# Optimization experiments

Measured on AMD Instinct MI355X. Metric: run time of the kernel, lower is better.

## Reference

```python
import jax, jax.numpy as jnp
import numpy as np
from jax.scipy.special import gammaln, digamma, logsumexp

# Gauss-Legendre quadrature on [0, 0.5] for the regularized incomplete beta
# I_{0.5}(a, b) = (1/B(a,b)) * int_0^{0.5} t^{a-1} (1-t)^{b-1} dt
_Q = 256
_gx, _gw = np.polynomial.legendre.leggauss(_Q)
_T_NP = 0.25 * (_gx + 1.0)          # nodes mapped to (0, 0.5)
_LOGW_NP = np.log(0.25 * _gw)       # log of scaled weights (half-length 0.25)


def betainc_half(a, b):
    """Regularized incomplete beta I_{0.5}(a, b), vectorized over leading dims.
    Evaluated in log-space via fixed Gauss-Legendre quadrature so it is smooth
    and differentiable in (a, b) (mirrors the custom BetaInc.apply autograd op).
    a, b: [...] positive floats. Returns [...].
    """
    t = jnp.asarray(_T_NP, dtype=a.dtype)        # [Q]
    logw = jnp.asarray(_LOGW_NP, dtype=a.dtype)  # [Q]
    # [..., Q] log integrand
    log_int = logw + (a[..., None] - 1.0) * jnp.log(t) \
                   + (b[..., None] - 1.0) * jnp.log1p(-t)
    log_B = gammaln(a) + gammaln(b) - gammaln(a + b)
    return jnp.exp(logsumexp(log_int, axis=-1) - log_B)


def setup_inputs() -> dict:
    key = jax.random.key(0)
    k1, k2, k3 = jax.random.split(key, 3)
    B, V = 65536, 512
    post_log = 0.1 * jax.random.normal(k1, (V,), dtype=jnp.float32)  # post_ param
    prior = jnp.ones((V,), dtype=jnp.float32)                        # prior = 1.0
    out = (2 * jax.random.randint(k2, (B, V), 0, 2) - 1).astype(jnp.int32)  # voter preds in {-1,+1}
    y = (2 * jax.random.randint(k3, (B, 1), 0, 2) - 1).astype(jnp.int32)    # labels in {-1,+1}
    return {"post_log": post_log, "prior": prior, "out": out, "y": y}


def reference(post_log, prior, out, y):
    B = out.shape[0]
    post = jnp.exp(post_log)                      # [V]
    eq = (y == out).astype(post.dtype)            # [B, V]
    correct = eq @ post                           # sum of post where y == out
    wrong = (1.0 - eq) @ post                     # sum of post where y != out
    # exact margin: m = 1 - 2 * I_{0.5}(correct, wrong)
    margin = 1.0 - 2.0 * betainc_half(correct, wrong)[:, None]   # [B, 1]
    # KL(Dir(post) || Dir(prior))
    kl = gammaln(post.sum()) - gammaln(post).sum()
    kl = kl - (gammaln(prior.sum()) - gammaln(prior).sum())
    kl = kl + jnp.sum((post - prior) * (digamma(post) - digamma(post.sum())))
    # predict: one Dirichlet draw of voter weights, score per label in {-1, +1}
    mv_post = jax.random.dirichlet(jax.random.key(1), post).astype(post.dtype)  # [V]
    score_neg = ((out == -1).astype(post.dtype) @ mv_post)[:, None]  # [B, 1]
    score_pos = ((out == 1).astype(post.dtype) @ mv_post)[:, None]   # [B, 1]
    kl_col = kl * jnp.ones((B, 1), dtype=post.dtype)
    # columns: [margin, score(label=-1), score(label=+1), kl]
    return jnp.concatenate([margin, score_neg, score_pos, kl_col], axis=1)
```

## Files before the change

### kernel.cpp

```cpp
#include <hip/hip_runtime.h>
#include <math.h>


struct K2 { unsigned a, b; };

__device__ __forceinline__ unsigned rotl32(unsigned v, int r) {
  return (v << r) | (v >> (32 - r));
}

__device__ __forceinline__ K2 tf2x32(K2 k, unsigned x0, unsigned x1) {
  unsigned ks0 = k.a, ks1 = k.b, ks2 = k.a ^ k.b ^ 0x1BD11BDAu;
  x0 += ks0; x1 += ks1;
#define TF_ROUND(r) { x0 += x1; x1 = rotl32(x1, (r)); x1 ^= x0; }
  TF_ROUND(13) TF_ROUND(15) TF_ROUND(26) TF_ROUND(6)
  x0 += ks1; x1 += ks2 + 1u;
  TF_ROUND(17) TF_ROUND(29) TF_ROUND(16) TF_ROUND(24)
  x0 += ks2; x1 += ks0 + 2u;
  TF_ROUND(13) TF_ROUND(15) TF_ROUND(26) TF_ROUND(6)
  x0 += ks0; x1 += ks1 + 3u;
  TF_ROUND(17) TF_ROUND(29) TF_ROUND(16) TF_ROUND(24)
  x0 += ks1; x1 += ks2 + 4u;
  TF_ROUND(13) TF_ROUND(15) TF_ROUND(26) TF_ROUND(6)
  x0 += ks2; x1 += ks0 + 5u;
#undef TF_ROUND
  return {x0, x1};
}

__device__ __forceinline__ void split2f(K2& key, K2& sub) {
  K2 c = tf2x32(key, 0u, 0u);
  sub = tf2x32(key, 0u, 1u);
  key = c;
}

__device__ __forceinline__ void split3f(K2& key, K2& xk, K2& Uk) {
  K2 c = tf2x32(key, 0u, 0u);
  xk = tf2x32(key, 0u, 1u);
  Uk = tf2x32(key, 0u, 2u);
  key = c;
}

__device__ __forceinline__ K2 split512_at(K2 k, int i) {
  return tf2x32(k, 0u, (unsigned)i);
}

__device__ __forceinline__ unsigned rbits32(K2 k) {
  K2 r = tf2x32(k, 0u, 0u);
  return r.a ^ r.b;
}

__device__ __forceinline__ float bits_to_u01(unsigned bits) {
  unsigned fb = (bits >> 9) | 0x3F800000u;
  return __uint_as_float(fb) - 1.0f;
}

__device__ __forceinline__ float erfinv_xla(float x) {
#pragma clang fp contract(off)
  float w = -log1pf(-(x * x));
  float p;
  if (w < 5.0f) {
    w = w - 2.5f;
    p = 2.81022636e-08f;
    p = 3.43273939e-07f + p * w;
    p = -3.5233877e-06f + p * w;
    p = -4.39150654e-06f + p * w;
    p = 0.00021858087f + p * w;
    p = -0.00125372503f + p * w;
    p = -0.00417768164f + p * w;
    p = 0.246640727f + p * w;
    p = 1.50140941f + p * w;
  } else {
    w = sqrtf(w) - 3.0f;
    p = -0.000200214257f;
    p = 0.000100950558f + p * w;
    p = 0.00134934322f + p * w;
    p = -0.00367342844f + p * w;
    p = 0.00573950773f + p * w;
    p = -0.0076224613f + p * w;
    p = 0.00943887047f + p * w;
    p = 1.00167406f + p * w;
    p = 2.83297682f + p * w;
  }
  return p * x;
}

__device__ __forceinline__ float normal_from_key(K2 k) {
#pragma clang fp contract(off)
  const float lo = -0.99999994f;
  float f = bits_to_u01(rbits32(k));
  float u = f * 2.0f + lo;
  u = fmaxf(lo, u);
  return 1.41421356f * erfinv_xla(u);
}

__device__ float gamma_one_log(K2 key, float alpha) {
#pragma clang fp contract(off)
  float alpha_orig = alpha;
  bool boost = (alpha >= 1.0f);
  float al = boost ? alpha : (alpha + 1.0f);
  float d = al - 0.33333334f;
  float c = 0.33333334f / sqrtf(9.0f * d);
  K2 sub;
  split2f(key, sub);
  float u_boost = bits_to_u01(rbits32(sub));
  float X = 0.0f, V = 1.0f, U = 2.0f;
  while ((U >= 1.0f - 0.0331f * (X * X)) &&
         (logf(U) >= 0.5f * X + d * ((1.0f - V) + logf(V)))) {
    K2 xk, Uk;
    split3f(key, xk, Uk);
    float x = 0.0f, v = -1.0f;
    while (v <= 0.0f) {
      K2 s2;
      split2f(xk, s2);
      x = normal_from_key(s2);
      v = 1.0f + x * c;
    }
    X = x * x;
    V = (v * v) * v;
    U = bits_to_u01(rbits32(Uk));
  }
  float log_sample = logf(d) + logf(V);
  if (boost) return log_sample;
  return log_sample + log1pf(-u_boost) / alpha_orig;
}

__device__ __forceinline__ double digamma_d(double x) {
  double r = 0.0;
  while (x < 6.0) { r -= 1.0 / x; x += 1.0; }
  double f = 1.0 / (x * x);
  double ser = f * (1.0 / 12.0 -
               f * (1.0 / 120.0 -
               f * (1.0 / 252.0 -
               f * (1.0 / 240.0 -
               f * (1.0 / 132.0)))));
  return r + log(x) - 0.5 / x - ser;
}

__device__ __forceinline__ double lgamma_stir(double x) {
  double shift = 0.0;
  while (x < 8.0) { shift -= log(x); x += 1.0; }
  double f = 1.0 / (x * x);
  double ser = (1.0 / 12.0 -
               f * (1.0 / 360.0 -
               f * (1.0 / 1260.0 -
               f * (1.0 / 1680.0)))) / x;
  return shift + 0.918938533204672741780329736406 + (x - 0.5) * log(x) - x + ser;
}

__device__ double breduce_sum(double* sd, double v) {
  int t = threadIdx.x;
  sd[t] = v; __syncthreads();
  for (int s = 256; s > 0; s >>= 1) {
    if (t < s) sd[t] += sd[t + s];
    __syncthreads();
  }
  double r = sd[0]; __syncthreads();
  return r;
}

__device__ float breduce_maxf(float* sf, float v) {
  int t = threadIdx.x;
  sf[t] = v; __syncthreads();
  for (int s = 256; s > 0; s >>= 1) {
    if (t < s) sf[t] = fmaxf(sf[t], sf[t + s]);
    __syncthreads();
  }
  float r = sf[0]; __syncthreads();
  return r;
}

__device__ float breduce_sumf(float* sf, float v) {
  int t = threadIdx.x;
  sf[t] = v; __syncthreads();
  for (int s = 256; s > 0; s >>= 1) {
    if (t < s) sf[t] += sf[t + s];
    __syncthreads();
  }
  float r = sf[0]; __syncthreads();
  return r;
}

#define MTAB_N 16384

__global__ void __launch_bounds__(512) smv_setup_kernel(
    const float* __restrict__ post_log, const float* __restrict__ prior,
    unsigned char* __restrict__ ws) {
  double* wsd = (double*)ws;
  float* fbase = (float*)(ws + 64);
  float* postf = fbase;
  float* mvf = fbase + 512;
  float* mtab = fbase + 1792;
  int tid = threadIdx.x;
  __shared__ double sd[512];

  if (blockIdx.x == 0) {
    __shared__ float sf[512];
    float alpha = expf(post_log[tid]);
    postf[tid] = alpha;
    double p = (double)alpha;
    double S = breduce_sum(sd, p);

    K2 root = {0u, 1u};
    K2 kv = split512_at(root, tid);
    float lg = gamma_one_log(kv, alpha);
    float mx = breduce_maxf(sf, lg);
    float un = expf(lg - mx);
    float se = breduce_sumf(sf, un);
    float mvv = un / se;
    mvf[tid] = mvv;
    float mtot = breduce_sumf(sf, mvv);

    double pr = (double)prior[tid];
    double dgS = digamma_d(S);
    double t3 = (p - pr) * (digamma_d(p) - dgS);
    double sum_lgp = breduce_sum(sd, lgamma(p));
    double Spr = breduce_sum(sd, pr);
    double sum_lgpr = breduce_sum(sd, lgamma(pr));
    double sum_t3 = breduce_sum(sd, t3);
    if (tid == 0) {
      double kl = lgamma(S) - sum_lgp - (lgamma(Spr) - sum_lgpr) + sum_t3;
      wsd[0] = S;
      wsd[1] = lgamma(S);
      wsd[2] = kl;
      wsd[3] = (double)mtot;
    }
    return;
  }

  double S = breduce_sum(sd, (double)expf(post_log[tid]));
  double lgS = lgamma(S);

  __shared__ float slt[256], sl1t[256], slw[256];
  if (tid < 256) {
    const int n = 256;
    const double nn = (double)n;
    double th = M_PI * (tid + 0.75) / (nn + 0.5);
    double corr = 1.0 - 1.0 / (8.0 * nn * nn) + 1.0 / (8.0 * nn * nn * nn);
    double x = corr * cos(th);
    double p0 = 1.0, p1 = x;
    for (int k = 2; k <= n; ++k) {
      double pk = ((2.0 * k - 1.0) * x * p1 - (k - 1.0) * p0) / (double)k;
      p0 = p1; p1 = pk;
    }
    double dp = nn * (x * p1 - p0) / (x * x - 1.0);
    double dx = -p1 / dp;
    double d2p = (2.0 * x * dp - nn * (nn + 1.0) * p1) / (1.0 - x * x);
    double xn = x + dx;
    double dpn = dp + d2p * dx;
    double w = 2.0 / ((1.0 - xn * xn) * dpn * dpn);
    double t = 0.25 * (xn + 1.0);
    slt[tid] = (float)log(t);
    sl1t[tid] = (float)log1p(-t);
    slw[tid] = (float)log(0.25 * w);
  }
  __syncthreads();

  int idx = (blockIdx.x - 1) * 512 + tid;
  double ad = S * (double)idx / (double)(MTAB_N - 1);
  ad = fmin(fmax(ad, 0.05), S - 0.05);
  float a = (float)ad;
  float b = (float)(S - ad);
  float am1 = a - 1.0f, bm1 = b - 1.0f;

  float m = -1e30f, s = 0.0f;
  for (int q = 0; q < 256; ++q) {
    float le = slw[q] + am1 * slt[q] + bm1 * sl1t[q];
    if (le > m) {
      s = s * expf(m - le) + 1.0f;
      m = le;
    } else {
      s += expf(le - m);
    }
  }
  float lse = m + logf(s);
  double logB = lgamma_stir(ad) + lgamma_stir((double)(S - ad)) - lgS;
  double I = exp((double)lse - logB);
  mtab[idx] = (float)(1.0 - 2.0 * I);
}

__global__ void __launch_bounds__(512) smv_main_kernel(
    const int* __restrict__ vout, const int* __restrict__ y,
    const unsigned char* __restrict__ ws, float* __restrict__ dout, int B) {
  __shared__ float s_post[512], s_mv[512];
  const double* wsd = (const double*)ws;
  const float* fbase = (const float*)(ws + 64);
  const float* mtab = fbase + 1792;
  int tid = threadIdx.x;
  s_post[tid] = fbase[tid];
  s_mv[tid] = fbase[512 + tid];
  float Sf = (float)wsd[0];
  float Mtot = (float)wsd[3];
  float klf = (float)wsd[2];
  float scale = (float)(MTAB_N - 1) / Sf;
  __syncthreads();

  int wave = tid >> 6, lane = tid & 63;
  int r0 = (blockIdx.x * 8 + wave) * 4;
  if (r0 >= B) return;

  const int4* rp0 = (const int4*)(vout + (size_t)r0 * 512);
  const int4* rp1 = (const int4*)(vout + (size_t)min(r0 + 1, B - 1) * 512);
  const int4* rp2 = (const int4*)(vout + (size_t)min(r0 + 2, B - 1) * 512);
  const int4* rp3 = (const int4*)(vout + (size_t)min(r0 + 3, B - 1) * 512);

  int4 v00 = rp0[lane], v01 = rp0[64 + lane];
  int4 v10 = rp1[lane], v11 = rp1[64 + lane];
  int4 v20 = rp2[lane], v21 = rp2[64 + lane];
  int4 v30 = rp3[lane], v31 = rp3[64 + lane];

  float4 p0 = *(const float4*)&s_post[lane * 4];
  float4 m0 = *(const float4*)&s_mv[lane * 4];
  float4 p1 = *(const float4*)&s_post[256 + lane * 4];
  float4 m1 = *(const float4*)&s_mv[256 + lane * 4];

  float dP0 = 0.f, dM0 = 0.f, dP1 = 0.f, dM1 = 0.f;
  float dP2 = 0.f, dM2 = 0.f, dP3 = 0.f, dM3 = 0.f;

#define ACC(dP, dM, c, pp, mm)                        \
  {                                                   \
    float ox = (float)(c).x, oy = (float)(c).y,       \
          oz = (float)(c).z, ow = (float)(c).w;       \
    dP = fmaf(ox, (pp).x, dP); dM = fmaf(ox, (mm).x, dM); \
    dP = fmaf(oy, (pp).y, dP); dM = fmaf(oy, (mm).y, dM); \
    dP = fmaf(oz, (pp).z, dP); dM = fmaf(oz, (mm).z, dM); \
    dP = fmaf(ow, (pp).w, dP); dM = fmaf(ow, (mm).w, dM); \
  }
  ACC(dP0, dM0, v00, p0, m0) ACC(dP0, dM0, v01, p1, m1)
  ACC(dP1, dM1, v10, p0, m0) ACC(dP1, dM1, v11, p1, m1)
  ACC(dP2, dM2, v20, p0, m0) ACC(dP2, dM2, v21, p1, m1)
  ACC(dP3, dM3, v30, p0, m0) ACC(dP3, dM3, v31, p1, m1)
#undef ACC

#pragma unroll
  for (int m = 1; m < 64; m <<= 1) {
    dP0 += __shfl_xor(dP0, m); dM0 += __shfl_xor(dM0, m);
    dP1 += __shfl_xor(dP1, m); dM1 += __shfl_xor(dM1, m);
    dP2 += __shfl_xor(dP2, m); dM2 += __shfl_xor(dM2, m);
    dP3 += __shfl_xor(dP3, m); dM3 += __shfl_xor(dM3, m);
  }

  if (lane < 4) {
    int r = r0 + lane;
    if (r < B) {
      float dP = (lane == 0) ? dP0 : (lane == 1) ? dP1 : (lane == 2) ? dP2 : dP3;
      float dM = (lane == 0) ? dM0 : (lane == 1) ? dM1 : (lane == 2) ? dM2 : dM3;
      float cneg = (Sf - dP) * 0.5f;
      float mneg = (Mtot - dM) * 0.5f;
      int yr = y[r];
      float a = (yr == -1) ? cneg : (Sf - cneg);
      float x = a * scale;
      x = fminf(fmaxf(x, 0.0f), (float)(MTAB_N - 1) - 1.001f);
      int i = (int)x;
      float fr = x - (float)i;
      float t0 = mtab[i], t1 = mtab[i + 1];
      float margin = fmaf(fr, t1 - t0, t0);
      float4 o4 = make_float4(margin, mneg, 1.0f - mneg, klf);
      *(float4*)(dout + (size_t)r * 4) = o4;
    }
  }
}

extern "C" void kernel_launch(void* const* d_in, const int* in_sizes, int n_in,
                              void* d_out, int out_size, void* d_ws,
                              size_t ws_size, hipStream_t stream) {
  const float* post_log = (const float*)d_in[0];
  const float* prior = (const float*)d_in[1];
  const int* vout = (const int*)d_in[2];
  const int* y = (const int*)d_in[3];
  float* dout = (float*)d_out;
  int B = in_sizes[3];
  unsigned char* ws = (unsigned char*)d_ws;

  hipLaunchKernelGGL(smv_setup_kernel, dim3(1 + MTAB_N / 512), dim3(512), 0,
                     stream, post_log, prior, ws);
  int blocks = (B + 31) / 32;
  hipLaunchKernelGGL(smv_main_kernel, dim3(blocks), dim3(512), 0, stream,
                     vout, y, ws, dout, B);
}
```

Baseline: 73.17 us.

## Speed up table build loops and cut wave reduction shuffles

The Legendre recurrence now multiplies by precomputed reciprocals held in shared memory instead of dividing in double precision. The online log-sum-exp becomes a two-pass max-then-sum with four independent accumulators, which removes the branchy rescaling at the cost of evaluating each term twice. In the main kernel the eight row and mv partial sums go through a transpose-style reduction: three xor stages on all eight values, then a single value per lane for the remaining stages. The four labels are also fetched with one vectorized load up front. The y load reads four ints from r0 with no bound check, so it relies on B being a multiple of 4.

```diff
diff --git a/kernel.cpp b/kernel.cpp
--- a/kernel.cpp
+++ b/kernel.cpp
@@ -226,6 +226,8 @@
     return;
   }
 
+  __shared__ double sinv[257];
+  if (tid < 256) sinv[tid + 1] = 1.0 / (double)(tid + 1);
   double S = breduce_sum(sd, (double)expf(post_log[tid]));
   double lgS = lgamma(S);
 
@@ -238,7 +240,7 @@
     double x = corr * cos(th);
     double p0 = 1.0, p1 = x;
     for (int k = 2; k <= n; ++k) {
-      double pk = ((2.0 * k - 1.0) * x * p1 - (k - 1.0) * p0) / (double)k;
+      double pk = ((2.0 * k - 1.0) * x * p1 - (k - 1.0) * p0) * sinv[k];
       p0 = p1; p1 = pk;
     }
     double dp = nn * (x * p1 - p0) / (x * x - 1.0);
@@ -261,17 +263,24 @@
   float b = (float)(S - ad);
   float am1 = a - 1.0f, bm1 = b - 1.0f;
 
-  float m = -1e30f, s = 0.0f;
-  for (int q = 0; q < 256; ++q) {
-    float le = slw[q] + am1 * slt[q] + bm1 * sl1t[q];
-    if (le > m) {
-      s = s * expf(m - le) + 1.0f;
-      m = le;
-    } else {
-      s += expf(le - m);
-    }
-  }
-  float lse = m + logf(s);
+  float m0 = -1e30f, m1 = -1e30f, m2 = -1e30f, m3 = -1e30f;
+#pragma unroll 4
+  for (int q = 0; q < 256; q += 4) {
+    m0 = fmaxf(m0, slw[q + 0] + am1 * slt[q + 0] + bm1 * sl1t[q + 0]);
+    m1 = fmaxf(m1, slw[q + 1] + am1 * slt[q + 1] + bm1 * sl1t[q + 1]);
+    m2 = fmaxf(m2, slw[q + 2] + am1 * slt[q + 2] + bm1 * sl1t[q + 2]);
+    m3 = fmaxf(m3, slw[q + 3] + am1 * slt[q + 3] + bm1 * sl1t[q + 3]);
+  }
+  float m = fmaxf(fmaxf(m0, m1), fmaxf(m2, m3));
+  float s0 = 0.f, s1 = 0.f, s2 = 0.f, s3 = 0.f;
+#pragma unroll 4
+  for (int q = 0; q < 256; q += 4) {
+    s0 += expf(slw[q + 0] + am1 * slt[q + 0] + bm1 * sl1t[q + 0] - m);
+    s1 += expf(slw[q + 1] + am1 * slt[q + 1] + bm1 * sl1t[q + 1] - m);
+    s2 += expf(slw[q + 2] + am1 * slt[q + 2] + bm1 * sl1t[q + 2] - m);
+    s3 += expf(slw[q + 3] + am1 * slt[q + 3] + bm1 * sl1t[q + 3] - m);
+  }
+  float lse = m + logf((s0 + s1) + (s2 + s3));
   double logB = lgamma_stir(ad) + lgamma_stir((double)(S - ad)) - lgS;
   double I = exp((double)lse - logB);
   mtab[idx] = (float)(1.0 - 2.0 * I);
@@ -306,6 +315,7 @@
   int4 v10 = rp1[lane], v11 = rp1[64 + lane];
   int4 v20 = rp2[lane], v21 = rp2[64 + lane];
   int4 v30 = rp3[lane], v31 = rp3[64 + lane];
+  int4 yv = *(const int4*)(y + r0);
 
   float4 p0 = *(const float4*)&s_post[lane * 4];
   float4 m0 = *(const float4*)&s_mv[lane * 4];
@@ -331,21 +341,31 @@
 #undef ACC
 
 #pragma unroll
-  for (int m = 1; m < 64; m <<= 1) {
+  for (int m = 1; m < 8; m <<= 1) {
     dP0 += __shfl_xor(dP0, m); dM0 += __shfl_xor(dM0, m);
     dP1 += __shfl_xor(dP1, m); dM1 += __shfl_xor(dM1, m);
     dP2 += __shfl_xor(dP2, m); dM2 += __shfl_xor(dM2, m);
     dP3 += __shfl_xor(dP3, m); dM3 += __shfl_xor(dM3, m);
   }
+  int g = lane & 7;
+  float v = dP0;
+  v = (g == 1) ? dP1 : v;
+  v = (g == 2) ? dP2 : v;
+  v = (g == 3) ? dP3 : v;
+  v = (g == 4) ? dM0 : v;
+  v = (g == 5) ? dM1 : v;
+  v = (g == 6) ? dM2 : v;
+  v = (g == 7) ? dM3 : v;
+#pragma unroll
+  for (int m = 8; m < 64; m <<= 1) v += __shfl_xor(v, m);
+  float vM = __shfl_xor(v, 4);
 
   if (lane < 4) {
     int r = r0 + lane;
     if (r < B) {
-      float dP = (lane == 0) ? dP0 : (lane == 1) ? dP1 : (lane == 2) ? dP2 : dP3;
-      float dM = (lane == 0) ? dM0 : (lane == 1) ? dM1 : (lane == 2) ? dM2 : dM3;
-      float cneg = (Sf - dP) * 0.5f;
-      float mneg = (Mtot - dM) * 0.5f;
-      int yr = y[r];
+      float cneg = (Sf - v) * 0.5f;
+      float mneg = (Mtot - vM) * 0.5f;
+      int yr = (lane == 0) ? yv.x : (lane == 1) ? yv.y : (lane == 2) ? yv.z : yv.w;
       float a = (yr == -1) ? cneg : (Sf - cneg);
       float x = a * scale;
       x = fminf(fmaxf(x, 0.0f), (float)(MTAB_N - 1) - 1.001f);
```

Result: faster. 60.91 us (-16.8%).
